# Kernel tuning notes

Measured on AMD Instinct MI355X. Metric: run time of the kernel, lower is better.

Reference implementation:

```python
import jax, jax.numpy as jnp
import numpy as np

B, N, H = 16, 1024, 768
NEG_INF = -9e15
SLOPE = 0.2


def setup_inputs() -> dict:
    key = jax.random.key(0)
    k1, k2, k3, k4, k5 = jax.random.split(key, 5)
    x = jax.random.normal(k1, (B, N, H), dtype=jnp.float32)
    # node_length acts as a per-node validity mask (float, used via outer product)
    lengths = jax.random.randint(k2, (B,), N // 2, N)
    node_length = (jnp.arange(N)[None, :] < lengths[:, None]).astype(jnp.float32)
    # sparse-ish binary adjacency with self-loops
    adj = (jax.random.uniform(k3, (B, N, N)) < 0.05).astype(jnp.float32)
    adj = jnp.maximum(adj, jnp.eye(N, dtype=jnp.float32)[None])
    # params: kaiming-normal init
    W = jax.random.normal(k4, (H, H), dtype=jnp.float32) * np.sqrt(2.0 / H)
    a = jax.random.normal(k5, (2 * H, 1), dtype=jnp.float32) * np.sqrt(2.0 / (2 * H))
    return {"input": x, "node_length": node_length, "graph_structure": adj, "W": W, "a": a}


def reference(input, node_length, graph_structure, W, a):
    # node_vec = A @ X  [B,N,H]
    node_vec = jnp.matmul(graph_structure, input)
    h = jnp.matmul(node_vec, W)  # [B,N,F]
    F_ = W.shape[1]
    a1 = a[:F_, 0]   # weights on h_i
    a2 = a[F_:, 0]   # weights on h_j
    # e[b,i,j] = leaky_relu(h_i . a1 + h_j . a2)  (identical to concat+matmul with a)
    s1 = jnp.einsum("bnf,f->bn", h, a1)
    s2 = jnp.einsum("bnf,f->bn", h, a2)
    e = jax.nn.leaky_relu(s1[:, :, None] + s2[:, None, :], negative_slope=SLOPE)
    # bias = outer product of node_length; mask where adj or bias <= 1e-6
    bias = node_length[:, :, None] * node_length[:, None, :]
    valid = (graph_structure > 1e-6) & (bias > 1e-6)
    scores = jnp.where(valid, e, NEG_INF)
    attn = jax.nn.softmax(scores, axis=-1)  # attn_dropout=0 -> identity
    return node_vec, attn
```

## Files before the change

kernel.cpp:

```cpp
#include <hip/hip_runtime.h>
#include <hip/hip_bf16.h>

#define BB 16
#define NN 1024
#define HH 768
#define NEG_INF_ -9.0e15f
#define SLOPE_ 0.2f

typedef __bf16 bh8 __attribute__((ext_vector_type(8)));
typedef __bf16 bh4 __attribute__((ext_vector_type(4)));
typedef float f4 __attribute__((ext_vector_type(4)));
typedef unsigned int u32;
typedef unsigned long long u64;


__device__ __forceinline__ float wave_sum0(float v) {
    #pragma unroll
    for (int off = 32; off > 0; off >>= 1) v += __shfl_down(v, off, 64);
    return v;
}
__device__ __forceinline__ float wave_sum_all(float v) {
    #pragma unroll
    for (int off = 1; off < 64; off <<= 1) v += __shfl_xor(v, off, 64);
    return v;
}
__device__ __forceinline__ float wave_max_all(float v) {
    #pragma unroll
    for (int off = 1; off < 64; off <<= 1) v = fmaxf(v, __shfl_xor(v, off, 64));
    return v;
}


__device__ __forceinline__ void gl_lds16(const void* g, void* l) {
    __builtin_amdgcn_global_load_lds(
        (const __attribute__((address_space(1))) u32*)g,
        (__attribute__((address_space(3))) u32*)l, 16, 0, 0);
}


__global__ __launch_bounds__(256) void wa_kernel(const float* __restrict__ W,
                                                 const float* __restrict__ a,
                                                 float* __restrict__ wa1,
                                                 float* __restrict__ wa2,
                                                 float* __restrict__ t1,
                                                 float* __restrict__ t2) {
    const int gid = blockIdx.x * 256 + threadIdx.x;
    if (gid < BB * NN) { t1[gid] = 0.f; t2[gid] = 0.f; }

    const int f = blockIdx.x * 4 + (threadIdx.x >> 6);
    const int lane = threadIdx.x & 63;
    const float* Wr = W + (size_t)f * HH;
    float v1 = 0.f, v2 = 0.f;
    #pragma unroll
    for (int i = 0; i < 3; i++) {
        const int h = lane * 4 + i * 256;
        const float4 w  = *(const float4*)(Wr + h);
        const float4 a1 = *(const float4*)(a + h);
        const float4 a2 = *(const float4*)(a + HH + h);
        v1 += w.x * a1.x + w.y * a1.y + w.z * a1.z + w.w * a1.w;
        v2 += w.x * a2.x + w.y * a2.y + w.z * a2.z + w.w * a2.w;
    }
    v1 = wave_sum0(v1);
    v2 = wave_sum0(v2);
    if (lane == 0) { wa1[f] = v1; wa2[f] = v2; }
}


__global__ __launch_bounds__(256) void xt_kernel(const float* __restrict__ x,
                                                 const float* __restrict__ wa1,
                                                 const float* __restrict__ wa2,
                                                 __bf16* __restrict__ xT,
                                                 float* __restrict__ t1,
                                                 float* __restrict__ t2) {
    __shared__ __bf16 T[32][36];
    const int b = blockIdx.z, nt = blockIdx.y, ht = blockIdx.x;
    const int t = threadIdx.x;
    const int r = t >> 3;
    const int c = (t & 7) * 4;
    const float4 v = *(const float4*)(x + ((size_t)b * NN + nt * 32 + r) * HH + ht * 32 + c);
    T[r][c + 0] = (__bf16)v.x; T[r][c + 1] = (__bf16)v.y;
    T[r][c + 2] = (__bf16)v.z; T[r][c + 3] = (__bf16)v.w;

    const float4 w1 = *(const float4*)(wa1 + ht * 32 + c);
    const float4 w2 = *(const float4*)(wa2 + ht * 32 + c);
    float p1 = v.x * w1.x + v.y * w1.y + v.z * w1.z + v.w * w1.w;
    float p2 = v.x * w2.x + v.y * w2.y + v.z * w2.z + v.w * w2.w;
    p1 += __shfl_down(p1, 4, 8); p1 += __shfl_down(p1, 2, 8); p1 += __shfl_down(p1, 1, 8);
    p2 += __shfl_down(p2, 4, 8); p2 += __shfl_down(p2, 2, 8); p2 += __shfl_down(p2, 1, 8);
    if ((t & 7) == 0) {
        atomicAdd(&t1[b * NN + nt * 32 + r], p1);
        atomicAdd(&t2[b * NN + nt * 32 + r], p2);
    }

    __syncthreads();
    const int h = t >> 3;
    const int nc = (t & 7) * 4;
    bh4 o = { T[nc + 0][h], T[nc + 1][h], T[nc + 2][h], T[nc + 3][h] };
    *(bh4*)(xT + ((size_t)b * HH + ht * 32 + h) * NN + nt * 32 + nc) = o;
}


__global__ __launch_bounds__(256) void s_pack_kernel(const float* __restrict__ adj,
                                                     const float* __restrict__ t1,
                                                     const float* __restrict__ t2,
                                                     float* __restrict__ s1,
                                                     float* __restrict__ s2,
                                                     u64* __restrict__ bits) {
    const int row = blockIdx.x * 4 + (threadIdx.x >> 6);
    const int lane = threadIdx.x & 63;
    const int b = row >> 10;
    const float* ar = adj + (size_t)row * NN;
    const float* t1b = t1 + b * NN;
    const float* t2b = t2 + b * NN;
    float v1 = 0.f, v2 = 0.f;
    const int seg = lane >> 4;
    const int sh = (lane & 15) * 4;
    #pragma unroll
    for (int i = 0; i < 4; i++) {
        const int j = lane * 4 + i * 256;
        const float4 av = *(const float4*)(ar + j);
        const float4 w1 = *(const float4*)(t1b + j);
        const float4 w2 = *(const float4*)(t2b + j);
        v1 += av.x * w1.x + av.y * w1.y + av.z * w1.z + av.w * w1.w;
        v2 += av.x * w2.x + av.y * w2.y + av.z * w2.z + av.w * w2.w;
        u32 nib = (av.x > 1e-6f ? 1u : 0u) | (av.y > 1e-6f ? 2u : 0u)
                | (av.z > 1e-6f ? 4u : 0u) | (av.w > 1e-6f ? 8u : 0u);
        u64 word = (u64)nib << sh;
        word |= __shfl_xor(word, 8, 16);
        word |= __shfl_xor(word, 4, 16);
        word |= __shfl_xor(word, 2, 16);
        word |= __shfl_xor(word, 1, 16);
        if ((lane & 15) == 0) bits[(size_t)row * 16 + i * 4 + seg] = word;
    }
    v1 = wave_sum0(v1);
    v2 = wave_sum0(v2);
    if (lane == 0) { s1[row] = v1; s2[row] = v2; }
}


#define BW 17

__global__ __launch_bounds__(256) void tail_kernel(const u64* __restrict__ bits,
                                                   const __bf16* __restrict__ xT,
                                                   float* __restrict__ out,
                                                   const float* __restrict__ nl,
                                                   const float* __restrict__ s1,
                                                   const float* __restrict__ s2,
                                                   float* __restrict__ attn) {
    __shared__ __bf16 LUT[256 * 8];
    __shared__ u64 bitsL[128 * BW];
    __shared__ __bf16 Bs[2][128 * 64];

    const int g = blockIdx.x;
    const int grp = g / 19;
    const int gm = g - grp * 19;
    const int tid = threadIdx.x, lane = tid & 63, wave = tid >> 6;

    if (gm < 3) {
        const int gg = grp * 3 + gm;
        const int bn = gg % 6;
        const int bm = (gg / 6) & 7;
        const int b  = gg / 48;
        const int wr = (wave >> 1) << 6;
        const int wc = (wave & 1) << 6;
        const int quad = lane >> 4, l16 = lane & 15;

        {
            bh8 e;
            #pragma unroll
            for (int j = 0; j < 8; j++) e[j] = ((tid >> j) & 1) ? (__bf16)1.0f : (__bf16)0.0f;
            *(bh8*)&LUT[tid * 8] = e;
        }
        {
            const u64* bg = bits + ((size_t)b * NN + bm * 128) * 16;
            #pragma unroll
            for (int q = 0; q < 8; q++) {
                const int gw = tid * 8 + q;
                bitsL[(gw >> 4) * BW + (gw & 15)] = bg[gw];
            }
        }

        const __bf16* Xb = xT + ((size_t)b * HH + bn * 128) * NN;

        f4 acc[4][4];
        #pragma unroll
        for (int i = 0; i < 4; i++)
            #pragma unroll
            for (int j = 0; j < 4; j++)
                acc[i][j] = (f4){0.f, 0.f, 0.f, 0.f};

        #pragma unroll
        for (int it = 0; it < 4; it++) {
            const int c = tid + 256 * it;
            const int r = c >> 3, j = c & 7, kc = j ^ (r & 7);
            gl_lds16(Xb + (size_t)r * NN + kc * 8, &Bs[0][r * 64 + j * 8]);
        }
        __syncthreads();

        for (int w = 0; w < 16; ++w) {
            const int cur = w & 1;
            if (w < 15) {
                const int kt = (w + 1) << 6;
                #pragma unroll
                for (int it = 0; it < 4; it++) {
                    const int c = tid + 256 * it;
                    const int r = c >> 3, j = c & 7, kc = j ^ (r & 7);
                    gl_lds16(Xb + (size_t)r * NN + kt + kc * 8, &Bs[cur ^ 1][r * 64 + j * 8]);
                }
            }

            u64 aw[4];
            #pragma unroll
            for (int i = 0; i < 4; i++)
                aw[i] = bitsL[(wr + i * 16 + l16) * BW + w];

            #pragma unroll
            for (int s = 0; s < 2; s++) {
                bh8 af[4], bf_[4];
                #pragma unroll
                for (int i = 0; i < 4; i++) {
                    const u32 byte = (u32)(aw[i] >> ((s * 4 + quad) * 8)) & 0xffu;
                    af[i] = *(const bh8*)&LUT[byte * 8];
                }
                #pragma unroll
                for (int j = 0; j < 4; j++) {
                    const int row = wc + j * 16 + l16;
                    const int jj = (s * 4 + quad) ^ (row & 7);
                    bf_[j] = *(const bh8*)&Bs[cur][row * 64 + jj * 8];
                }
                #pragma unroll
                for (int i = 0; i < 4; i++)
                    #pragma unroll
                    for (int j = 0; j < 4; j++)
                        acc[i][j] = __builtin_amdgcn_mfma_f32_16x16x32_bf16(af[i], bf_[j], acc[i][j], 0, 0, 0);
            }
            __syncthreads();
        }

        float* Cb = out + (size_t)b * NN * HH + (size_t)bm * 128 * HH + bn * 128;
        const int rbase = wr + quad * 4;
        const int cbase = wc + l16;
        #pragma unroll
        for (int i = 0; i < 4; i++)
            #pragma unroll
            for (int j = 0; j < 4; j++)
                #pragma unroll
                for (int r = 0; r < 4; r++)
                    Cb[(size_t)(rbase + i * 16 + r) * HH + cbase + j * 16] = acc[i][j][r];
    } else {
        const int sg = grp * 16 + (gm - 3);
        const int row = sg * 4 + wave;
        const int b = row >> 10, n = row & (NN - 1);
        const u64* bwr = bits + (size_t)row * 16;
        const float* nlb = nl + (size_t)b * NN;
        const float* s2b = s2 + (size_t)b * NN;
        const float s1v = s1[row];
        const bool rowok = nlb[n] > 1e-6f;
        const int bitbase = (lane & 15) * 4;

        f4 sc[4];
        float mx = NEG_INF_;
        #pragma unroll
        for (int i = 0; i < 4; i++) {
            const int j = lane * 4 + i * 256;
            const float4 sv = *(const float4*)(s2b + j);
            const float4 nv = *(const float4*)(nlb + j);
            const u64 w64 = bwr[i * 4 + (lane >> 4)];
            const float zs[4] = { s1v + sv.x, s1v + sv.y, s1v + sv.z, s1v + sv.w };
            const float ns[4] = { nv.x, nv.y, nv.z, nv.w };
            #pragma unroll
            for (int e = 0; e < 4; e++) {
                const float z = zs[e];
                const float lr = z > 0.f ? z : SLOPE_ * z;
                const bool valid = rowok && ((w64 >> (bitbase + e)) & 1ull) && (ns[e] > 1e-6f);
                sc[i][e] = valid ? lr : NEG_INF_;
                mx = fmaxf(mx, sc[i][e]);
            }
        }
        mx = wave_max_all(mx);

        f4 ex[4];
        float sum = 0.f;
        #pragma unroll
        for (int i = 0; i < 4; i++)
            #pragma unroll
            for (int e = 0; e < 4; e++) {
                ex[i][e] = __expf(sc[i][e] - mx);
                sum += ex[i][e];
            }
        sum = wave_sum_all(sum);
        const float inv = 1.0f / sum;

        float* outr = attn + (size_t)row * NN;
        #pragma unroll
        for (int i = 0; i < 4; i++) {
            const int j = lane * 4 + i * 256;
            float4 o;
            o.x = ex[i][0] * inv; o.y = ex[i][1] * inv;
            o.z = ex[i][2] * inv; o.w = ex[i][3] * inv;
            *(float4*)(outr + j) = o;
        }
    }
}


extern "C" void kernel_launch(void* const* d_in, const int* in_sizes, int n_in,
                              void* d_out, int out_size, void* d_ws, size_t ws_size,
                              hipStream_t stream) {
    const float* x   = (const float*)d_in[0];
    const float* nl  = (const float*)d_in[1];
    const float* adj = (const float*)d_in[2];
    const float* W   = (const float*)d_in[3];
    const float* a   = (const float*)d_in[4];

    float* out = (float*)d_out;
    float* node_vec = out;
    float* attn = out + (size_t)BB * NN * HH;

    char* wsb = (char*)d_ws;
    float* wa1 = (float*)(wsb);
    float* wa2 = wa1 + HH;
    float* t1  = wa2 + HH;
    float* t2  = t1 + BB * NN;
    float* s1  = t2 + BB * NN;
    float* s2  = s1 + BB * NN;
    u64*    bits = (u64*)(wsb + (1u << 20));
    __bf16* xT   = (__bf16*)(wsb + (4u << 20));

    hipLaunchKernelGGL(wa_kernel, dim3(192), dim3(256), 0, stream, W, a, wa1, wa2, t1, t2);
    hipLaunchKernelGGL(xt_kernel, dim3(24, 32, BB), dim3(256), 0, stream, x, wa1, wa2, xT, t1, t2);
    hipLaunchKernelGGL(s_pack_kernel, dim3(4096), dim3(256), 0, stream, adj, t1, t2, s1, s2, bits);
    hipLaunchKernelGGL(tail_kernel, dim3(19 * 256), dim3(256), 0, stream, bits, xT, node_vec, nl, s1, s2, attn);
}
```

Before: 274.7 us.

## Fuse GEMM and softmax into persistent blocks with interleaved softmax ordering

```diff
diff --git a/kernel.cpp b/kernel.cpp
--- a/kernel.cpp
+++ b/kernel.cpp
@@ -138,118 +138,14 @@
 }
 
 
-#define BW 17
-
-__global__ __launch_bounds__(256) void tail_kernel(const u64* __restrict__ bits,
-                                                   const __bf16* __restrict__ xT,
-                                                   float* __restrict__ out,
-                                                   const float* __restrict__ nl,
-                                                   const float* __restrict__ s1,
-                                                   const float* __restrict__ s2,
-                                                   float* __restrict__ attn) {
-    __shared__ __bf16 LUT[256 * 8];
-    __shared__ u64 bitsL[128 * BW];
-    __shared__ __bf16 Bs[2][128 * 64];
-
-    const int g = blockIdx.x;
-    const int grp = g / 19;
-    const int gm = g - grp * 19;
-    const int tid = threadIdx.x, lane = tid & 63, wave = tid >> 6;
-
-    if (gm < 3) {
-        const int gg = grp * 3 + gm;
-        const int bn = gg % 6;
-        const int bm = (gg / 6) & 7;
-        const int b  = gg / 48;
-        const int wr = (wave >> 1) << 6;
-        const int wc = (wave & 1) << 6;
-        const int quad = lane >> 4, l16 = lane & 15;
-
-        {
-            bh8 e;
-            #pragma unroll
-            for (int j = 0; j < 8; j++) e[j] = ((tid >> j) & 1) ? (__bf16)1.0f : (__bf16)0.0f;
-            *(bh8*)&LUT[tid * 8] = e;
-        }
-        {
-            const u64* bg = bits + ((size_t)b * NN + bm * 128) * 16;
-            #pragma unroll
-            for (int q = 0; q < 8; q++) {
-                const int gw = tid * 8 + q;
-                bitsL[(gw >> 4) * BW + (gw & 15)] = bg[gw];
-            }
-        }
-
-        const __bf16* Xb = xT + ((size_t)b * HH + bn * 128) * NN;
-
-        f4 acc[4][4];
-        #pragma unroll
-        for (int i = 0; i < 4; i++)
-            #pragma unroll
-            for (int j = 0; j < 4; j++)
-                acc[i][j] = (f4){0.f, 0.f, 0.f, 0.f};
-
-        #pragma unroll
-        for (int it = 0; it < 4; it++) {
-            const int c = tid + 256 * it;
-            const int r = c >> 3, j = c & 7, kc = j ^ (r & 7);
-            gl_lds16(Xb + (size_t)r * NN + kc * 8, &Bs[0][r * 64 + j * 8]);
-        }
-        __syncthreads();
-
-        for (int w = 0; w < 16; ++w) {
-            const int cur = w & 1;
-            if (w < 15) {
-                const int kt = (w + 1) << 6;
-                #pragma unroll
-                for (int it = 0; it < 4; it++) {
-                    const int c = tid + 256 * it;
-                    const int r = c >> 3, j = c & 7, kc = j ^ (r & 7);
-                    gl_lds16(Xb + (size_t)r * NN + kt + kc * 8, &Bs[cur ^ 1][r * 64 + j * 8]);
-                }
-            }
-
-            u64 aw[4];
-            #pragma unroll
-            for (int i = 0; i < 4; i++)
-                aw[i] = bitsL[(wr + i * 16 + l16) * BW + w];
-
-            #pragma unroll
-            for (int s = 0; s < 2; s++) {
-                bh8 af[4], bf_[4];
-                #pragma unroll
-                for (int i = 0; i < 4; i++) {
-                    const u32 byte = (u32)(aw[i] >> ((s * 4 + quad) * 8)) & 0xffu;
-                    af[i] = *(const bh8*)&LUT[byte * 8];
-                }
-                #pragma unroll
-                for (int j = 0; j < 4; j++) {
-                    const int row = wc + j * 16 + l16;
-                    const int jj = (s * 4 + quad) ^ (row & 7);
-                    bf_[j] = *(const bh8*)&Bs[cur][row * 64 + jj * 8];
-                }
-                #pragma unroll
-                for (int i = 0; i < 4; i++)
-                    #pragma unroll
-                    for (int j = 0; j < 4; j++)
-                        acc[i][j] = __builtin_amdgcn_mfma_f32_16x16x32_bf16(af[i], bf_[j], acc[i][j], 0, 0, 0);
-            }
-            __syncthreads();
-        }
-
-        float* Cb = out + (size_t)b * NN * HH + (size_t)bm * 128 * HH + bn * 128;
-        const int rbase = wr + quad * 4;
-        const int cbase = wc + l16;
-        #pragma unroll
-        for (int i = 0; i < 4; i++)
-            #pragma unroll
-            for (int j = 0; j < 4; j++)
-                #pragma unroll
-                for (int r = 0; r < 4; r++)
-                    Cb[(size_t)(rbase + i * 16 + r) * HH + cbase + j * 16] = acc[i][j][r];
-    } else {
-        const int sg = grp * 16 + (gm - 3);
-        const int row = sg * 4 + wave;
+__device__ __forceinline__ void softmax_rows(int g, int wave, int lane,
+                                             const u64* __restrict__ bits,
+                                             const float* __restrict__ nl,
+                                             const float* __restrict__ s1,
+                                             const float* __restrict__ s2,
+                                             float* __restrict__ attn) {
+    for (int rg = g; rg < 4096; rg += 768) {
+        const int row = rg * 4 + wave;
         const int b = row >> 10, n = row & (NN - 1);
         const u64* bwr = bits + (size_t)row * 16;
         const float* nlb = nl + (size_t)b * NN;
@@ -301,6 +197,116 @@
             *(float4*)(outr + j) = o;
         }
     }
+}
+
+
+__global__ __launch_bounds__(256) void gemm_sm_kernel(const u64* __restrict__ bits,
+                                                      const __bf16* __restrict__ xT,
+                                                      float* __restrict__ out,
+                                                      const float* __restrict__ nl,
+                                                      const float* __restrict__ s1,
+                                                      const float* __restrict__ s2,
+                                                      float* __restrict__ attn) {
+    __shared__ __bf16 LUT[256 * 8];
+    __shared__ __bf16 Bs[2][128 * 64];
+
+    const int g = blockIdx.x;
+    const int tid = threadIdx.x, lane = tid & 63, wave = tid >> 6;
+
+    {
+        bh8 e;
+        #pragma unroll
+        for (int j = 0; j < 8; j++) e[j] = ((tid >> j) & 1) ? (__bf16)1.0f : (__bf16)0.0f;
+        *(bh8*)&LUT[tid * 8] = e;
+    }
+
+    if (g & 1) softmax_rows(g, wave, lane, bits, nl, s1, s2, attn);
+
+    const int bn = g % 6;
+    const int bm = (g / 6) & 7;
+    const int b  = g / 48;
+    const int wr = (wave >> 1) << 6;
+    const int wc = (wave & 1) << 6;
+    const int quad = lane >> 4, l16 = lane & 15;
+
+    const __bf16* Xb = xT + ((size_t)b * HH + bn * 128) * NN;
+    const u64* bgA = bits + ((size_t)b * NN + bm * 128) * 16;
+
+    f4 acc[4][4];
+    #pragma unroll
+    for (int i = 0; i < 4; i++)
+        #pragma unroll
+        for (int j = 0; j < 4; j++)
+            acc[i][j] = (f4){0.f, 0.f, 0.f, 0.f};
+
+    u64 awc[4];
+    #pragma unroll
+    for (int i = 0; i < 4; i++)
+        awc[i] = bgA[(size_t)(wr + i * 16 + l16) * 16 + 0];
+
+    #pragma unroll
+    for (int it = 0; it < 4; it++) {
+        const int c = tid + 256 * it;
+        const int r = c >> 3, j = c & 7, kc = j ^ (r & 7);
+        gl_lds16(Xb + (size_t)r * NN + kc * 8, &Bs[0][r * 64 + j * 8]);
+    }
+    __syncthreads();
+
+    for (int w = 0; w < 16; ++w) {
+        const int cur = w & 1;
+        u64 awn[4];
+        if (w < 15) {
+            const int kt = (w + 1) << 6;
+            #pragma unroll
+            for (int it = 0; it < 4; it++) {
+                const int c = tid + 256 * it;
+                const int r = c >> 3, j = c & 7, kc = j ^ (r & 7);
+                gl_lds16(Xb + (size_t)r * NN + kt + kc * 8, &Bs[cur ^ 1][r * 64 + j * 8]);
+            }
+            #pragma unroll
+            for (int i = 0; i < 4; i++)
+                awn[i] = bgA[(size_t)(wr + i * 16 + l16) * 16 + w + 1];
+        }
+
+        #pragma unroll
+        for (int s = 0; s < 2; s++) {
+            bh8 af[4], bf_[4];
+            #pragma unroll
+            for (int i = 0; i < 4; i++) {
+                const u32 byte = (u32)(awc[i] >> ((s * 4 + quad) * 8)) & 0xffu;
+                af[i] = *(const bh8*)&LUT[byte * 8];
+            }
+            #pragma unroll
+            for (int j = 0; j < 4; j++) {
+                const int row = wc + j * 16 + l16;
+                const int jj = (s * 4 + quad) ^ (row & 7);
+                bf_[j] = *(const bh8*)&Bs[cur][row * 64 + jj * 8];
+            }
+            #pragma unroll
+            for (int i = 0; i < 4; i++)
+                #pragma unroll
+                for (int j = 0; j < 4; j++)
+                    acc[i][j] = __builtin_amdgcn_mfma_f32_16x16x32_bf16(af[i], bf_[j], acc[i][j], 0, 0, 0);
+        }
+        __syncthreads();
+        if (w < 15) {
+            #pragma unroll
+            for (int i = 0; i < 4; i++) awc[i] = awn[i];
+        }
+    }
+
+    float* Cb = out + (size_t)b * NN * HH + (size_t)bm * 128 * HH + bn * 128;
+    const int rbase = wr + quad * 4;
+    const int cbase = wc + l16;
+    #pragma unroll
+    for (int i = 0; i < 4; i++)
+        #pragma unroll
+        for (int j = 0; j < 4; j++)
+            #pragma unroll
+            for (int r = 0; r < 4; r++)
+                Cb[(size_t)(rbase + i * 16 + r) * HH + cbase + j * 16] = acc[i][j][r];
+
+    if (!(g & 1)) softmax_rows(g, wave, lane, bits, nl, s1, s2, attn);
 }
 
 
@@ -330,5 +336,5 @@
     hipLaunchKernelGGL(wa_kernel, dim3(192), dim3(256), 0, stream, W, a, wa1, wa2, t1, t2);
     hipLaunchKernelGGL(xt_kernel, dim3(24, 32, BB), dim3(256), 0, stream, x, wa1, wa2, xT, t1, t2);
     hipLaunchKernelGGL(s_pack_kernel, dim3(4096), dim3(256), 0, stream, adj, t1, t2, s1, s2, bits);
-    hipLaunchKernelGGL(tail_kernel, dim3(19 * 256), dim3(256), 0, stream, bits, xT, node_vec, nl, s1, s2, attn);
-}
+    hipLaunchKernelGGL(gemm_sm_kernel, dim3(768), dim3(256), 0, stream, bits, xT, node_vec, nl, s1, s2, attn);
+}
```

Measured after the change: 283.7 us. 1.03x slower.
